# Optimization experiments

Measured on AMD Instinct MI355X. Metric: run time of the kernel, lower is better.

## Reference

```python
import jax, jax.numpy as jnp
import numpy as np

B, H, W, DIM = 8, 64, 64, 256
HEADS, DH = 8, 64
HID = HEADS * DH  # 512
EPS = 1e-5


def setup_inputs() -> dict:
    key = jax.random.key(0)
    k0, k1, k2 = jax.random.split(key, 3)
    return {
        "x": jax.random.normal(k0, (B, H, W, DIM), dtype=jnp.float32),
        "w_qkv": jax.random.normal(k1, (DIM, 3 * HID), dtype=jnp.float32) / np.sqrt(DIM),
        "gn_scale": jnp.ones((HID,), jnp.float32),
        "gn_bias": jnp.zeros((HID,), jnp.float32),
        "w_out": jax.random.normal(k2, (HID, DIM), dtype=jnp.float32) / np.sqrt(HID),
        "b_out": jnp.zeros((DIM,), jnp.float32),
    }


def reference(x, w_qkv, gn_scale, gn_bias, w_out, b_out):
    b, h, w, c = x.shape
    n = h * w
    scale = DH ** -0.5
    # 1x1 conv (no bias) == channel matmul
    qkv = jnp.einsum('bxyc,cf->bxyf', x, w_qkv)
    q, k, v = jnp.split(qkv, 3, axis=-1)
    # 'b x y (h c) -> b h c (x y)'
    to_heads = lambda t: t.reshape(b, n, HEADS, DH).transpose(0, 2, 3, 1)
    q, k, v = map(to_heads, (q, k, v))  # [b, heads, d, n]
    q = jax.nn.softmax(q, axis=-2) * scale  # softmax over feature dim d
    k = jax.nn.softmax(k, axis=-1)          # softmax over token dim n
    context = jnp.einsum('bhdn,bhen->bhde', k, v)   # small d x e context
    out = jnp.einsum('bhde,bhdn->bhen', context, q)  # [b, heads, e, n]
    # 'b h c (x y) -> b x y (h c)'
    out = out.transpose(0, 3, 1, 2).reshape(b, h, w, HID)
    # GroupNorm with 1 group: normalize over (H, W, C) per sample
    mu = out.mean(axis=(1, 2, 3), keepdims=True)
    var = out.var(axis=(1, 2, 3), keepdims=True)
    out = (out - mu) * jax.lax.rsqrt(var + EPS) * gn_scale + gn_bias
    # final 1x1 conv with bias
    return jnp.einsum('bxyf,fc->bxyc', out, w_out) + b_out
```

## Files before the change

kernel.cpp:

```cpp
#include <hip/hip_runtime.h>


typedef unsigned short ushort_t;
typedef __attribute__((ext_vector_type(8))) short short8;
typedef __attribute__((ext_vector_type(4))) float floatx4;

__device__ __forceinline__ float b2f(ushort_t u) {
  unsigned int i = ((unsigned int)u) << 16;
  float f;
  __builtin_memcpy(&f, &i, 4);
  return f;
}
__device__ __forceinline__ ushort_t f2b(float f) {
  unsigned int i;
  __builtin_memcpy(&i, &f, 4);
  unsigned int r = (i + 0x7FFFu + ((i >> 16) & 1u)) >> 16;
  return (ushort_t)r;
}

__device__ __forceinline__ void load_lds16(const ushort_t* g, ushort_t* l) {
  __builtin_amdgcn_global_load_lds(
      (const __attribute__((address_space(1))) unsigned int*)g,
      (__attribute__((address_space(3))) unsigned int*)l, 16, 0, 0);
}

__global__ __launch_bounds__(256) void cast_f32_bf16(
    const float* __restrict__ in, ushort_t* __restrict__ out) {
  long i = ((long)blockIdx.x * 256 + threadIdx.x) * 4;
  float4 v = *(const float4*)(in + i);
  ushort4 o;
  o.x = f2b(v.x);
  o.y = f2b(v.y);
  o.z = f2b(v.z);
  o.w = f2b(v.w);
  *(ushort4*)(out + i) = o;
}

__global__ __launch_bounds__(256) void transpose_f32_bf16(
    const float* __restrict__ in, ushort_t* __restrict__ out, int R, int C,
    const float* __restrict__ scale) {
  __shared__ ushort_t t[32][33];
  int c0 = blockIdx.x * 32, r0 = blockIdx.y * 32;
  int tx = threadIdx.x & 31, ty = threadIdx.x >> 5;
  for (int i = 0; i < 32; i += 8) {
    float s = scale ? scale[r0 + ty + i] : 1.0f;
    t[ty + i][tx] = f2b(in[(long)(r0 + ty + i) * C + c0 + tx] * s);
  }
  __syncthreads();
  for (int i = 0; i < 32; i += 8)
    out[(long)(c0 + ty + i) * R + r0 + tx] = t[tx][ty + i];
}

__global__ __launch_bounds__(64) void prep_gw_kernel(
    const float* __restrict__ gn_scale, const float* __restrict__ gn_bias,
    const float* __restrict__ w_out, const float* __restrict__ b_out,
    float* __restrict__ gw1, float* __restrict__ bias2) {
  int c = blockIdx.x * 64 + threadIdx.x;
  float g1 = 0.f, b2 = 0.f;
  for (int f = 0; f < 512; ++f) {
    float w = w_out[f * 256 + c];
    g1 += gn_scale[f] * w;
    b2 += gn_bias[f] * w;
  }
  gw1[c] = g1;
  bias2[c] = b2 + b_out[c];
}

template <int MODE, bool SWAP>
__global__ __launch_bounds__(256) void gemm_tpl(
    const ushort_t* __restrict__ A, const ushort_t* __restrict__ Bt,
    void* __restrict__ Cv, int M, int K, int F,
    const float* __restrict__ murs, const float* __restrict__ gw1,
    const float* __restrict__ bias2) {
  __shared__ __align__(16) ushort_t As[128][32];
  __shared__ __align__(16) ushort_t Bs[128][32];
  int tid = threadIdx.x;
  long m0 = (long)(SWAP ? blockIdx.y : blockIdx.x) * 128;
  long f0 = (long)(SWAP ? blockIdx.x : blockIdx.y) * 128;
  int wv = tid >> 6, lane = tid & 63;
  int wm = wv & 1, wf = wv >> 1;
  int l15 = lane & 15, quad = lane >> 4;

  floatx4 acc[4][4];
  floatx4 zero = {0.f, 0.f, 0.f, 0.f};
  for (int i = 0; i < 4; i++)
    for (int j = 0; j < 4; j++) acc[i][j] = zero;

  for (int k0 = 0; k0 < K; k0 += 32) {
    __syncthreads();
#pragma unroll
    for (int r = 0; r < 2; ++r) {
      int chunk = r * 256 + tid;
      int row = chunk >> 2;
      int kc = chunk & 3;
      load_lds16(A + (m0 + row) * (long)K + k0 + kc * 8, &As[row][kc * 8]);
      load_lds16(Bt + (f0 + row) * (long)K + k0 + kc * 8, &Bs[row][kc * 8]);
    }
    __syncthreads();
    short8 af[4], bfr[4];
#pragma unroll
    for (int mt = 0; mt < 4; mt++)
      af[mt] = *(const short8*)(&As[wm * 64 + mt * 16 + l15][quad * 8]);
#pragma unroll
    for (int ft = 0; ft < 4; ft++)
      bfr[ft] = *(const short8*)(&Bs[wf * 64 + ft * 16 + l15][quad * 8]);
#pragma unroll
    for (int mt = 0; mt < 4; mt++)
#pragma unroll
      for (int ft = 0; ft < 4; ft++)
        acc[mt][ft] = __builtin_amdgcn_mfma_f32_16x16x32_bf16(
            af[mt], bfr[ft], acc[mt][ft], 0, 0, 0);
  }

  {
    float* C = (float*)Cv;
    int b = (int)(m0 >> 12);
    float mu = murs[b * 2], rs = murs[b * 2 + 1];
#pragma unroll
    for (int mt = 0; mt < 4; mt++)
#pragma unroll
      for (int ft = 0; ft < 4; ft++) {
        long col = f0 + wf * 64 + ft * 16 + l15;
        float c1 = bias2[col] - rs * mu * gw1[col];
#pragma unroll
        for (int r = 0; r < 4; r++) {
          long row = m0 + wm * 64 + mt * 16 + quad * 4 + r;
          C[row * F + col] = rs * acc[mt][ft][r] + c1;
        }
      }
  }
}

__global__ __launch_bounds__(256, 4) void kvctx_kernel(
    const ushort_t* __restrict__ xb, const ushort_t* __restrict__ wqkvT,
    float* __restrict__ ctxP, float* __restrict__ ksumP) {
  __shared__ __align__(16) char lds[32768];
  ushort_t* kTs = (ushort_t*)lds;
  ushort_t* vTs = (ushort_t*)(lds + 16384);

  int gid = blockIdx.x;
  int h = gid >> 8;
  int c0i = gid & 255;
  int b = c0i >> 5;
  int cy = c0i & 31;
  int bh = b * 8 + h;
  int tid = threadIdx.x, wv = tid >> 6, lane = tid & 63;
  int wm = wv & 1, wfk = wv >> 1;
  int l15 = lane & 15, quad = lane >> 4;
  long m0 = (long)b * 4096 + cy * 128;

  floatx4 zero = {0.f, 0.f, 0.f, 0.f};
  floatx4 acc[4][4];
  for (int i = 0; i < 4; i++)
    for (int j = 0; j < 4; j++) acc[i][j] = zero;

  auto stage = [&](int p, int k0) {
    ushort_t* Ab = (ushort_t*)(lds + p * 16384);
    ushort_t* Bb = Ab + 4096;
#pragma unroll
    for (int r = 0; r < 2; ++r) {
      int chunk = r * 256 + tid;
      int row = chunk >> 2, kc = chunk & 3;
      int gc = kc ^ (row & 3);
      long arow = (row < 64 ? 512 : 960) + h * 64 + row;
      load_lds16(wqkvT + arow * 256 + k0 + gc * 8, Ab + chunk * 8);
      load_lds16(xb + (m0 + row) * 256 + k0 + gc * 8, Bb + chunk * 8);
    }
  };

  stage(0, 0);
  __syncthreads();
#pragma unroll
  for (int t = 0; t < 8; ++t) {
    int p = t & 1;
    if (t < 7) stage(p ^ 1, (t + 1) * 32);
    ushort_t* Ab = (ushort_t*)(lds + p * 16384);
    ushort_t* Bb = Ab + 4096;
    short8 af[4], bfr[4];
#pragma unroll
    for (int mt = 0; mt < 4; mt++) {
      int row = wfk * 64 + mt * 16 + l15;
      int slot = quad ^ (row & 3);
      af[mt] = *(const short8*)(Ab + row * 32 + slot * 8);
    }
#pragma unroll
    for (int ft = 0; ft < 4; ft++) {
      int rowb = wm * 64 + ft * 16 + l15;
      int slot = quad ^ (rowb & 3);
      bfr[ft] = *(const short8*)(Bb + rowb * 32 + slot * 8);
    }
#pragma unroll
    for (int mt = 0; mt < 4; mt++)
#pragma unroll
      for (int ft = 0; ft < 4; ft++)
        acc[mt][ft] = __builtin_amdgcn_mfma_f32_16x16x32_bf16(
            af[mt], bfr[ft], acc[mt][ft], 0, 0, 0);
    __syncthreads();
  }

  {
    ushort_t* T = wfk ? vTs : kTs;
#pragma unroll
    for (int mt = 0; mt < 4; mt++)
#pragma unroll
      for (int ft = 0; ft < 4; ft++) {
        int n = wm * 64 + ft * 16 + l15;
        int c = n >> 3, u = n & 7;
#pragma unroll
        for (int r = 0; r < 4; r++) {
          int d = mt * 16 + quad * 4 + r;
          float v = acc[mt][ft][r];
          if (!wfk) v = __expf(v);
          int slot = (c & 8) | ((c ^ d) & 7);
          T[d * 128 + slot * 8 + u] = f2b(v);
        }
      }
  }
  __syncthreads();

  floatx4 cacc[4], acc1;
  for (int i = 0; i < 4; i++) cacc[i] = zero;
  acc1 = zero;
  short8 ones;
#pragma unroll
  for (int u = 0; u < 8; ++u) ones[u] = (short)0x3F80;
#pragma unroll
  for (int ks = 0; ks < 4; ++ks) {
    int d = wv * 16 + l15;
    int cidx = ks * 4 + quad;
    int sa = (cidx & 8) | ((cidx ^ d) & 7);
    short8 a = *(const short8*)(kTs + d * 128 + sa * 8);
    short8 bf[4];
#pragma unroll
    for (int ft = 0; ft < 4; ++ft) {
      int e = ft * 16 + l15;
      int sb = (cidx & 8) | ((cidx ^ e) & 7);
      bf[ft] = *(const short8*)(vTs + e * 128 + sb * 8);
    }
#pragma unroll
    for (int ft = 0; ft < 4; ++ft)
      cacc[ft] = __builtin_amdgcn_mfma_f32_16x16x32_bf16(a, bf[ft], cacc[ft],
                                                         0, 0, 0);
    acc1 = __builtin_amdgcn_mfma_f32_16x16x32_bf16(a, ones, acc1, 0, 0, 0);
  }
  float* cb = ctxP + ((long)cy * 64 + bh) * 4096;
#pragma unroll
  for (int ft = 0; ft < 4; ++ft)
    *(floatx4*)&cb[(ft * 16 + l15) * 64 + wv * 16 + quad * 4] = cacc[ft];
  if (l15 == 0) {
    float* kb = ksumP + ((long)cy * 64 + bh) * 64;
    *(floatx4*)&kb[wv * 16 + quad * 4] = acc1;
  }
}

__global__ __launch_bounds__(256) void reduce_kernel(
    const float* __restrict__ ctxP, const float* __restrict__ ksumP,
    ushort_t* __restrict__ ctxB) {
  int bid = blockIdx.x;
  int bh = bid >> 4;
  int j = (bid & 15) * 256 + threadIdx.x;
  int e = j >> 6, d = j & 63;
  float ks = 0.f;
#pragma unroll
  for (int c = 0; c < 32; ++c) ks += ksumP[((long)c * 64 + bh) * 64 + d];
  float s = 0.f;
#pragma unroll
  for (int c = 0; c < 32; ++c) s += ctxP[((long)c * 64 + bh) * 4096 + j];
  int slot = (d >> 3) ^ (e & 7);
  ctxB[(long)bh * 4096 + e * 64 + slot * 8 + (d & 7)] = f2b(s / ks);
}

__global__ __launch_bounds__(256, 4) void qattn_kernel(
    const ushort_t* __restrict__ xb, const ushort_t* __restrict__ wqT,
    const ushort_t* __restrict__ ctxB, ushort_t* __restrict__ A2,
    float* __restrict__ gstats) {
  __shared__ __align__(16) char lds[32800];
  ushort_t* P = (ushort_t*)lds;
  ushort_t* Od = (ushort_t*)lds;
  float* red = (float*)(lds + 32768);

  int tid = threadIdx.x;
  int bx = blockIdx.x, by = blockIdx.y;
  long m0 = (long)bx * 128;
  long f0 = (long)by * 128;
  int wv = tid >> 6, lane = tid & 63;
  int wm = wv & 1, wf = wv >> 1;
  int l15 = lane & 15, quad = lane >> 4;
  int b = bx >> 5;

  floatx4 acc[4][4];
  floatx4 zero = {0.f, 0.f, 0.f, 0.f};
  for (int i = 0; i < 4; i++)
    for (int j = 0; j < 4; j++) acc[i][j] = zero;

  auto stage = [&](int p, int k0) {
    ushort_t* Ab = (ushort_t*)(lds + p * 16384);
    ushort_t* Bb = Ab + 4096;
#pragma unroll
    for (int r = 0; r < 2; ++r) {
      int chunk = r * 256 + tid;
      int row = chunk >> 2, kc = chunk & 3;
      int gc = kc ^ (row & 3);
      load_lds16(xb + (m0 + row) * 256 + k0 + gc * 8, Ab + chunk * 8);
      load_lds16(wqT + (f0 + row) * 256 + k0 + gc * 8, Bb + chunk * 8);
    }
  };

  stage(0, 0);
  __syncthreads();
#pragma unroll
  for (int t = 0; t < 8; ++t) {
    int p = t & 1;
    if (t < 7) stage(p ^ 1, (t + 1) * 32);
    ushort_t* Ab = (ushort_t*)(lds + p * 16384);
    ushort_t* Bb = Ab + 4096;
    short8 af[4], bfr[4];
#pragma unroll
    for (int mt = 0; mt < 4; mt++) {
      int row = wm * 64 + mt * 16 + l15;
      int slot = quad ^ (row & 3);
      af[mt] = *(const short8*)(Ab + row * 32 + slot * 8);
    }
#pragma unroll
    for (int ft = 0; ft < 4; ft++) {
      int rowb = wf * 64 + ft * 16 + l15;
      int slot = quad ^ (rowb & 3);
      bfr[ft] = *(const short8*)(Bb + rowb * 32 + slot * 8);
    }
#pragma unroll
    for (int mt = 0; mt < 4; mt++)
#pragma unroll
      for (int ft = 0; ft < 4; ft++)
        acc[mt][ft] = __builtin_amdgcn_mfma_f32_16x16x32_bf16(
            af[mt], bfr[ft], acc[mt][ft], 0, 0, 0);
    __syncthreads();
  }

  const ushort_t* cg = ctxB + ((long)(b * 8 + by * 2 + wf)) * 4096;
  short8 cfr0[4];
#pragma unroll
  for (int ft = 0; ft < 4; ++ft) {
    int e = ft * 16 + l15;
    int slot = quad ^ (e & 7);
    cfr0[ft] = *(const short8*)(cg + e * 64 + slot * 8);
  }

  float rs[4][4];
#pragma unroll
  for (int mt = 0; mt < 4; mt++)
#pragma unroll
    for (int r = 0; r < 4; r++) rs[mt][r] = 0.f;
#pragma unroll
  for (int mt = 0; mt < 4; mt++)
#pragma unroll
    for (int ft = 0; ft < 4; ft++)
#pragma unroll
      for (int r = 0; r < 4; r++) {
        float e = __expf(acc[mt][ft][r]);
        acc[mt][ft][r] = e;
        rs[mt][r] += e;
      }
#pragma unroll
  for (int mt = 0; mt < 4; mt++)
#pragma unroll
    for (int r = 0; r < 4; r++) {
      float t = rs[mt][r];
      t += __shfl_xor(t, 1);
      t += __shfl_xor(t, 2);
      t += __shfl_xor(t, 4);
      t += __shfl_xor(t, 8);
      rs[mt][r] = 0.125f / t;
    }

  {
    ushort_t* Pw = P + wf * 8192;
#pragma unroll
    for (int mt = 0; mt < 4; mt++)
#pragma unroll
      for (int ft = 0; ft < 4; ft++) {
        int d = ft * 16 + l15;
#pragma unroll
        for (int r = 0; r < 4; r++) {
          int row = wm * 64 + mt * 16 + quad * 4 + r;
          int slot = (d >> 3) ^ (row & 7);
          Pw[row * 64 + slot * 8 + (d & 7)] = f2b(acc[mt][ft][r] * rs[mt][r]);
        }
      }
  }

  short8 cfr1[4];
#pragma unroll
  for (int ft = 0; ft < 4; ++ft) {
    int e = ft * 16 + l15;
    int slot = (4 + quad) ^ (e & 7);
    cfr1[ft] = *(const short8*)(cg + e * 64 + slot * 8);
  }

  floatx4 o[4][4];
  for (int i = 0; i < 4; i++)
    for (int j = 0; j < 4; j++) o[i][j] = zero;
  {
    const ushort_t* Pr = P + wf * 8192;
    short8 af[4];
#pragma unroll
    for (int mt = 0; mt < 4; mt++) {
      int row = wm * 64 + mt * 16 + l15;
      int slot = quad ^ (row & 7);
      af[mt] = *(const short8*)(Pr + row * 64 + slot * 8);
    }
#pragma unroll
    for (int mt = 0; mt < 4; mt++)
#pragma unroll
      for (int ft = 0; ft < 4; ft++)
        o[mt][ft] = __builtin_amdgcn_mfma_f32_16x16x32_bf16(af[mt], cfr0[ft],
                                                            o[mt][ft], 0, 0,
                                                            0);
#pragma unroll
    for (int mt = 0; mt < 4; mt++) {
      int row = wm * 64 + mt * 16 + l15;
      int slot = (4 + quad) ^ (row & 7);
      af[mt] = *(const short8*)(Pr + row * 64 + slot * 8);
    }
#pragma unroll
    for (int mt = 0; mt < 4; mt++)
#pragma unroll
      for (int ft = 0; ft < 4; ft++)
        o[mt][ft] = __builtin_amdgcn_mfma_f32_16x16x32_bf16(af[mt], cfr1[ft],
                                                            o[mt][ft], 0, 0,
                                                            0);
  }

  float lsum = 0.f, lss = 0.f;
#pragma unroll
  for (int mt = 0; mt < 4; mt++)
#pragma unroll
    for (int ft = 0; ft < 4; ft++)
#pragma unroll
      for (int r = 0; r < 4; r++) {
        float v = o[mt][ft][r];
        lsum += v;
        lss += v * v;
      }

  __syncthreads();

#pragma unroll
  for (int mt = 0; mt < 4; mt++)
#pragma unroll
    for (int ft = 0; ft < 4; ft++) {
      int cl = wf * 64 + ft * 16 + l15;
      int c = cl >> 3, u = cl & 7;
#pragma unroll
      for (int r = 0; r < 4; r++) {
        int rl = wm * 64 + mt * 16 + quad * 4 + r;
        int slot = (c & 8) | ((c ^ rl) & 7);
        Od[rl * 128 + slot * 8 + u] = f2b(o[mt][ft][r]);
      }
    }
  __syncthreads();

  {
    ushort_t* a2g = A2 + m0 * 512 + f0;
#pragma unroll
    for (int s = 0; s < 8; ++s) {
      int off = s * 2048 + tid * 8;
      int row = off >> 7;
      int c2 = (off & 127) >> 3;
      int slot = (c2 & 8) | ((c2 ^ row) & 7);
      *(short8*)(a2g + (long)row * 512 + c2 * 8) =
          *(const short8*)(Od + row * 128 + slot * 8);
    }
  }

  for (int s = 32; s > 0; s >>= 1) {
    lsum += __shfl_xor(lsum, s);
    lss += __shfl_xor(lss, s);
  }
  if (lane == 0) {
    red[wv * 2] = lsum;
    red[wv * 2 + 1] = lss;
  }
  __syncthreads();
  if (tid == 0) {
    float a = 0.f, c = 0.f;
    for (int w2 = 0; w2 < 4; w2++) {
      a += red[w2 * 2];
      c += red[w2 * 2 + 1];
    }
    atomicAdd(&gstats[b * 2], a);
    atomicAdd(&gstats[b * 2 + 1], c);
  }
}

__global__ __launch_bounds__(64) void finalize_murs(
    const float* __restrict__ gstats, float* __restrict__ murs) {
  int tid = threadIdx.x;
  if (tid < 8) {
    float cnt = 4096.f * 512.f;
    float mu = gstats[tid * 2] / cnt;
    float var = gstats[tid * 2 + 1] / cnt - mu * mu;
    murs[tid * 2] = mu;
    murs[tid * 2 + 1] = rsqrtf(var + 1e-5f);
  }
}

extern "C" void kernel_launch(void* const* d_in, const int* in_sizes, int n_in,
                              void* d_out, int out_size, void* d_ws,
                              size_t ws_size, hipStream_t stream) {
  const float* x = (const float*)d_in[0];
  const float* w_qkv = (const float*)d_in[1];
  const float* gn_scale = (const float*)d_in[2];
  const float* gn_bias = (const float*)d_in[3];
  const float* w_out = (const float*)d_in[4];
  const float* b_out = (const float*)d_in[5];
  float* out = (float*)d_out;

  char* w = (char*)d_ws;
  ushort_t* xb = (ushort_t*)(w + 0);
  ushort_t* A2 = (ushort_t*)(w + 16777216);
  float* ctxP = (float*)(w + 50331648);
  float* ksumP = (float*)(w + 83886080);
  ushort_t* wqkvT = (ushort_t*)(w + 84410368);
  ushort_t* w2T = (ushort_t*)(w + 85196800);
  ushort_t* ctxB = (ushort_t*)(w + 85458944);
  float* gstats = (float*)(w + 85983232);
  float* murs = (float*)(w + 85983296);
  float* bias2 = (float*)(w + 85983360);
  float* gw1 = (float*)(w + 85984384);

  hipMemsetAsync(gstats, 0, 64, stream);

  cast_f32_bf16<<<8388608 / 4 / 256, 256, 0, stream>>>(x, xb);
  transpose_f32_bf16<<<dim3(1536 / 32, 256 / 32), 256, 0, stream>>>(
      w_qkv, wqkvT, 256, 1536, nullptr);
  transpose_f32_bf16<<<dim3(256 / 32, 512 / 32), 256, 0, stream>>>(
      w_out, w2T, 512, 256, gn_scale);
  prep_gw_kernel<<<4, 64, 0, stream>>>(gn_scale, gn_bias, w_out, b_out, gw1,
                                       bias2);
  kvctx_kernel<<<2048, 256, 0, stream>>>(xb, wqkvT, ctxP, ksumP);
  reduce_kernel<<<1024, 256, 0, stream>>>(ctxP, ksumP, ctxB);
  qattn_kernel<<<dim3(256, 4), 256, 0, stream>>>(xb, wqkvT, ctxB, A2, gstats);
  finalize_murs<<<1, 64, 0, stream>>>(gstats, murs);
  gemm_tpl<2, false><<<dim3(256, 2), 256, 0, stream>>>(
      A2, w2T, out, 32768, 512, 256, murs, gw1, bias2);
}
```

Baseline: 233.4 us.

## Merge prep kernels, fold GN finalize into output GEMM, double-buffer with swizzle

Merges the cast, both weight transposes and the gn-weight prep into a single launch, which removes three kernel launches. It drops the finalize_murs kernel and has each output GEMM block compute mean and rstd from gstats directly. The output GEMM is rewritten with double-buffered LDS staging that overlaps the next K-tile load with the MFMAs, plus an XOR swizzle to reduce LDS bank conflicts. In exchange, each block recomputes the statistics, the GEMM uses more LDS, and it is hardcoded to K=512 and F=256.

```diff
diff --git a/kernel.cpp b/kernel.cpp
--- a/kernel.cpp
+++ b/kernel.cpp
@@ -24,38 +24,51 @@
       (__attribute__((address_space(3))) unsigned int*)l, 16, 0, 0);
 }
 
-__global__ __launch_bounds__(256) void cast_f32_bf16(
-    const float* __restrict__ in, ushort_t* __restrict__ out) {
-  long i = ((long)blockIdx.x * 256 + threadIdx.x) * 4;
-  float4 v = *(const float4*)(in + i);
-  ushort4 o;
-  o.x = f2b(v.x);
-  o.y = f2b(v.y);
-  o.z = f2b(v.z);
-  o.w = f2b(v.w);
-  *(ushort4*)(out + i) = o;
-}
-
-__global__ __launch_bounds__(256) void transpose_f32_bf16(
-    const float* __restrict__ in, ushort_t* __restrict__ out, int R, int C,
-    const float* __restrict__ scale) {
-  __shared__ ushort_t t[32][33];
-  int c0 = blockIdx.x * 32, r0 = blockIdx.y * 32;
-  int tx = threadIdx.x & 31, ty = threadIdx.x >> 5;
-  for (int i = 0; i < 32; i += 8) {
-    float s = scale ? scale[r0 + ty + i] : 1.0f;
-    t[ty + i][tx] = f2b(in[(long)(r0 + ty + i) * C + c0 + tx] * s);
-  }
-  __syncthreads();
-  for (int i = 0; i < 32; i += 8)
-    out[(long)(c0 + ty + i) * R + r0 + tx] = t[tx][ty + i];
-}
-
-__global__ __launch_bounds__(64) void prep_gw_kernel(
+__global__ __launch_bounds__(256) void prep_all(
+    const float* __restrict__ x, const float* __restrict__ w_qkv,
     const float* __restrict__ gn_scale, const float* __restrict__ gn_bias,
     const float* __restrict__ w_out, const float* __restrict__ b_out,
-    float* __restrict__ gw1, float* __restrict__ bias2) {
-  int c = blockIdx.x * 64 + threadIdx.x;
+    ushort_t* __restrict__ xb, ushort_t* __restrict__ wqkvT,
+    ushort_t* __restrict__ w2T, float* __restrict__ gw1,
+    float* __restrict__ bias2) {
+  __shared__ ushort_t t[32][33];
+  int bid = blockIdx.x;
+  if (bid < 8192) {
+    long i = ((long)bid * 256 + threadIdx.x) * 4;
+    float4 v = *(const float4*)(x + i);
+    ushort4 o;
+    o.x = f2b(v.x);
+    o.y = f2b(v.y);
+    o.z = f2b(v.z);
+    o.w = f2b(v.w);
+    *(ushort4*)(xb + i) = o;
+    return;
+  }
+  bid -= 8192;
+  if (bid < 384) {
+    int c0 = (bid % 48) * 32, r0 = (bid / 48) * 32;
+    int tx = threadIdx.x & 31, ty = threadIdx.x >> 5;
+    for (int i = 0; i < 32; i += 8)
+      t[ty + i][tx] = f2b(w_qkv[(long)(r0 + ty + i) * 1536 + c0 + tx]);
+    __syncthreads();
+    for (int i = 0; i < 32; i += 8)
+      wqkvT[(long)(c0 + ty + i) * 256 + r0 + tx] = t[tx][ty + i];
+    return;
+  }
+  bid -= 384;
+  if (bid < 128) {
+    int c0 = (bid % 8) * 32, r0 = (bid / 8) * 32;
+    int tx = threadIdx.x & 31, ty = threadIdx.x >> 5;
+    for (int i = 0; i < 32; i += 8) {
+      float s = gn_scale[r0 + ty + i];
+      t[ty + i][tx] = f2b(w_out[(long)(r0 + ty + i) * 256 + c0 + tx] * s);
+    }
+    __syncthreads();
+    for (int i = 0; i < 32; i += 8)
+      w2T[(long)(c0 + ty + i) * 512 + r0 + tx] = t[tx][ty + i];
+    return;
+  }
+  int c = threadIdx.x;
   float g1 = 0.f, b2 = 0.f;
   for (int f = 0; f < 512; ++f) {
     float w = w_out[f * 256 + c];
@@ -64,71 +77,6 @@
   }
   gw1[c] = g1;
   bias2[c] = b2 + b_out[c];
-}
-
-template <int MODE, bool SWAP>
-__global__ __launch_bounds__(256) void gemm_tpl(
-    const ushort_t* __restrict__ A, const ushort_t* __restrict__ Bt,
-    void* __restrict__ Cv, int M, int K, int F,
-    const float* __restrict__ murs, const float* __restrict__ gw1,
-    const float* __restrict__ bias2) {
-  __shared__ __align__(16) ushort_t As[128][32];
-  __shared__ __align__(16) ushort_t Bs[128][32];
-  int tid = threadIdx.x;
-  long m0 = (long)(SWAP ? blockIdx.y : blockIdx.x) * 128;
-  long f0 = (long)(SWAP ? blockIdx.x : blockIdx.y) * 128;
-  int wv = tid >> 6, lane = tid & 63;
-  int wm = wv & 1, wf = wv >> 1;
-  int l15 = lane & 15, quad = lane >> 4;
-
-  floatx4 acc[4][4];
-  floatx4 zero = {0.f, 0.f, 0.f, 0.f};
-  for (int i = 0; i < 4; i++)
-    for (int j = 0; j < 4; j++) acc[i][j] = zero;
-
-  for (int k0 = 0; k0 < K; k0 += 32) {
-    __syncthreads();
-#pragma unroll
-    for (int r = 0; r < 2; ++r) {
-      int chunk = r * 256 + tid;
-      int row = chunk >> 2;
-      int kc = chunk & 3;
-      load_lds16(A + (m0 + row) * (long)K + k0 + kc * 8, &As[row][kc * 8]);
-      load_lds16(Bt + (f0 + row) * (long)K + k0 + kc * 8, &Bs[row][kc * 8]);
-    }
-    __syncthreads();
-    short8 af[4], bfr[4];
-#pragma unroll
-    for (int mt = 0; mt < 4; mt++)
-      af[mt] = *(const short8*)(&As[wm * 64 + mt * 16 + l15][quad * 8]);
-#pragma unroll
-    for (int ft = 0; ft < 4; ft++)
-      bfr[ft] = *(const short8*)(&Bs[wf * 64 + ft * 16 + l15][quad * 8]);
-#pragma unroll
-    for (int mt = 0; mt < 4; mt++)
-#pragma unroll
-      for (int ft = 0; ft < 4; ft++)
-        acc[mt][ft] = __builtin_amdgcn_mfma_f32_16x16x32_bf16(
-            af[mt], bfr[ft], acc[mt][ft], 0, 0, 0);
-  }
-
-  {
-    float* C = (float*)Cv;
-    int b = (int)(m0 >> 12);
-    float mu = murs[b * 2], rs = murs[b * 2 + 1];
-#pragma unroll
-    for (int mt = 0; mt < 4; mt++)
-#pragma unroll
-      for (int ft = 0; ft < 4; ft++) {
-        long col = f0 + wf * 64 + ft * 16 + l15;
-        float c1 = bias2[col] - rs * mu * gw1[col];
-#pragma unroll
-        for (int r = 0; r < 4; r++) {
-          long row = m0 + wm * 64 + mt * 16 + quad * 4 + r;
-          C[row * F + col] = rs * acc[mt][ft][r] + c1;
-        }
-      }
-  }
 }
 
 __global__ __launch_bounds__(256, 4) void kvctx_kernel(
@@ -492,16 +440,82 @@
   }
 }
 
-__global__ __launch_bounds__(64) void finalize_murs(
-    const float* __restrict__ gstats, float* __restrict__ murs) {
+__global__ __launch_bounds__(256, 4) void gemm_out(
+    const ushort_t* __restrict__ A, const ushort_t* __restrict__ Bt,
+    float* __restrict__ C, const float* __restrict__ gstats,
+    const float* __restrict__ gw1, const float* __restrict__ bias2) {
+  __shared__ __align__(16) char lds[32768];
   int tid = threadIdx.x;
-  if (tid < 8) {
-    float cnt = 4096.f * 512.f;
-    float mu = gstats[tid * 2] / cnt;
-    float var = gstats[tid * 2 + 1] / cnt - mu * mu;
-    murs[tid * 2] = mu;
-    murs[tid * 2 + 1] = rsqrtf(var + 1e-5f);
-  }
+  long m0 = (long)blockIdx.x * 128;
+  long f0 = (long)blockIdx.y * 128;
+  int wv = tid >> 6, lane = tid & 63;
+  int wm = wv & 1, wf = wv >> 1;
+  int l15 = lane & 15, quad = lane >> 4;
+
+  floatx4 acc[4][4];
+  floatx4 zero = {0.f, 0.f, 0.f, 0.f};
+  for (int i = 0; i < 4; i++)
+    for (int j = 0; j < 4; j++) acc[i][j] = zero;
+
+  auto stage = [&](int p, int k0) {
+    ushort_t* Ab = (ushort_t*)(lds + p * 16384);
+    ushort_t* Bb = Ab + 4096;
+#pragma unroll
+    for (int r = 0; r < 2; ++r) {
+      int chunk = r * 256 + tid;
+      int row = chunk >> 2, kc = chunk & 3;
+      int gc = kc ^ (row & 3);
+      load_lds16(A + (m0 + row) * 512 + k0 + gc * 8, Ab + chunk * 8);
+      load_lds16(Bt + (f0 + row) * 512 + k0 + gc * 8, Bb + chunk * 8);
+    }
+  };
+
+  stage(0, 0);
+  __syncthreads();
+  for (int t = 0; t < 16; ++t) {
+    int p = t & 1;
+    if (t < 15) stage(p ^ 1, (t + 1) * 32);
+    ushort_t* Ab = (ushort_t*)(lds + p * 16384);
+    ushort_t* Bb = Ab + 4096;
+    short8 af[4], bfr[4];
+#pragma unroll
+    for (int mt = 0; mt < 4; mt++) {
+      int row = wm * 64 + mt * 16 + l15;
+      int slot = quad ^ (row & 3);
+      af[mt] = *(const short8*)(Ab + row * 32 + slot * 8);
+    }
+#pragma unroll
+    for (int ft = 0; ft < 4; ft++) {
+      int rowb = wf * 64 + ft * 16 + l15;
+      int slot = quad ^ (rowb & 3);
+      bfr[ft] = *(const short8*)(Bb + rowb * 32 + slot * 8);
+    }
+#pragma unroll
+    for (int mt = 0; mt < 4; mt++)
+#pragma unroll
+      for (int ft = 0; ft < 4; ft++)
+        acc[mt][ft] = __builtin_amdgcn_mfma_f32_16x16x32_bf16(
+            af[mt], bfr[ft], acc[mt][ft], 0, 0, 0);
+    __syncthreads();
+  }
+
+  int b = (int)(m0 >> 12);
+  float cnt = 4096.f * 512.f;
+  float mu = gstats[b * 2] / cnt;
+  float var = gstats[b * 2 + 1] / cnt - mu * mu;
+  float rsv = rsqrtf(var + 1e-5f);
+#pragma unroll
+  for (int mt = 0; mt < 4; mt++)
+#pragma unroll
+    for (int ft = 0; ft < 4; ft++) {
+      long col = f0 + wf * 64 + ft * 16 + l15;
+      float c1 = bias2[col] - rsv * mu * gw1[col];
+#pragma unroll
+      for (int r = 0; r < 4; r++) {
+        long row = m0 + wm * 64 + mt * 16 + quad * 4 + r;
+        C[row * 256 + col] = rsv * acc[mt][ft][r] + c1;
+      }
+    }
 }
 
 extern "C" void kernel_launch(void* const* d_in, const int* in_sizes, int n_in,
@@ -524,23 +538,16 @@
   ushort_t* w2T = (ushort_t*)(w + 85196800);
   ushort_t* ctxB = (ushort_t*)(w + 85458944);
   float* gstats = (float*)(w + 85983232);
-  float* murs = (float*)(w + 85983296);
   float* bias2 = (float*)(w + 85983360);
   float* gw1 = (float*)(w + 85984384);
 
   hipMemsetAsync(gstats, 0, 64, stream);
 
-  cast_f32_bf16<<<8388608 / 4 / 256, 256, 0, stream>>>(x, xb);
-  transpose_f32_bf16<<<dim3(1536 / 32, 256 / 32), 256, 0, stream>>>(
-      w_qkv, wqkvT, 256, 1536, nullptr);
-  transpose_f32_bf16<<<dim3(256 / 32, 512 / 32), 256, 0, stream>>>(
-      w_out, w2T, 512, 256, gn_scale);
-  prep_gw_kernel<<<4, 64, 0, stream>>>(gn_scale, gn_bias, w_out, b_out, gw1,
-                                       bias2);
+  prep_all<<<8705, 256, 0, stream>>>(x, w_qkv, gn_scale, gn_bias, w_out,
+                                     b_out, xb, wqkvT, w2T, gw1, bias2);
   kvctx_kernel<<<2048, 256, 0, stream>>>(xb, wqkvT, ctxP, ksumP);
   reduce_kernel<<<1024, 256, 0, stream>>>(ctxP, ksumP, ctxB);
   qattn_kernel<<<dim3(256, 4), 256, 0, stream>>>(xb, wqkvT, ctxB, A2, gstats);
-  finalize_murs<<<1, 64, 0, stream>>>(gstats, murs);
-  gemm_tpl<2, false><<<dim3(256, 2), 256, 0, stream>>>(
-      A2, w2T, out, 32768, 512, 256, murs, gw1, bias2);
-}
+  gemm_out<<<dim3(256, 2), 256, 0, stream>>>(A2, w2T, out, gstats, gw1,
+                                             bias2);
+}
```

New measurement: 221.2 us. -5.2%, faster.
